# Optimization experiments

Hardware: AMD Instinct MI355X
Metric: run time of the kernel (lower is better)

## Reference

```python
import jax, jax.numpy as jnp
import numpy as np

N = 50000   # num nodes
E = 800000  # num edges
D = 128     # in_features
C = 1.0     # curvature c
MIN_NORM = 1e-15
BALL_EPS = 4e-3  # float32 boundary eps in PoincareBall.proj


def setup_inputs() -> dict:
    key = jax.random.key(0)
    k1, k2 = jax.random.split(key)
    x = jax.random.normal(k1, (N, D), dtype=jnp.float32)
    edge_index = jax.random.randint(k2, (2, E), 0, N, dtype=jnp.int32)
    return {"x": x, "edge_index": edge_index}


def _expmap0(u, c):
    sqrt_c = c ** 0.5
    u_norm = jnp.maximum(jnp.linalg.norm(u, axis=-1, keepdims=True), MIN_NORM)
    return jnp.tanh(sqrt_c * u_norm) * u / (sqrt_c * u_norm)


def _proj(p, c):
    norm = jnp.maximum(jnp.linalg.norm(p, axis=-1, keepdims=True), MIN_NORM)
    maxnorm = (1.0 - BALL_EPS) / (c ** 0.5)
    return jnp.where(norm > maxnorm, p / norm * maxnorm, p)


def reference(x, edge_index):
    row, col = edge_index[0], edge_index[1]
    # add_remaining_self_loops: drop existing self-loops (weight->0), append N fresh self-loops w=1
    w = jnp.where(row == col, 0.0, 1.0).astype(x.dtype)
    loop = jnp.arange(N, dtype=row.dtype)
    row_f = jnp.concatenate([row, loop])
    col_f = jnp.concatenate([col, loop])
    w_f = jnp.concatenate([w, jnp.ones((N,), x.dtype)])
    # symmetric GCN normalization: D^{-1/2} A D^{-1/2}
    deg = jax.ops.segment_sum(w_f, row_f, num_segments=N)
    dis = jnp.where(deg > 0, 1.0 / jnp.sqrt(jnp.where(deg > 0, deg, 1.0)), 0.0)
    nw = dis[row_f] * w_f * dis[col_f]  # [E+N]
    # gather source features, weighted scatter-add into destination rows
    support = nw[:, None] * x[col_f]                       # [E+N, D]
    result = jax.ops.segment_sum(support, row_f, num_segments=N)  # [N, D]
    return _proj(_expmap0(result, C), C)
```

## Files before the change

### kernel.cpp

```cpp
#include <hip/hip_runtime.h>
#include <math.h>

#define N_NODES 50000
#define N_EDGES 800000
#define DFEAT   128
#define MAXNORM (1.0f - 4e-3f)
#define CAP     32
#define OVF_CAP 8192
#define NPART   8
#define PSIZE   (N_NODES / NPART)
#define SENT    N_NODES

typedef float vfloat4 __attribute__((ext_vector_type(4)));


__device__ __forceinline__ void build_edge(int r, int c, int lo, int hi,
                                           int* __restrict__ deg,
                                           unsigned short* __restrict__ adj16,
                                           int* __restrict__ ovf, int* __restrict__ ovf_cnt) {
    if (r < lo || r >= hi || r == c) return;
    int pos = atomicAdd(&deg[r], 1);
    if (pos < CAP) adj16[r * CAP + pos] = (unsigned short)c;
    else {
        int o = atomicAdd(ovf_cnt, 1);
        if (o < OVF_CAP) { ovf[2 * o] = r; ovf[2 * o + 1] = c; }
    }
}

__global__ void k_build(const int* __restrict__ row, const int* __restrict__ col,
                        int* __restrict__ deg, unsigned short* __restrict__ adj16,
                        int* __restrict__ ovf, int* __restrict__ ovf_cnt, int e) {
    int p      = blockIdx.x & (NPART - 1);
    int vblock = blockIdx.x >> 3;
    int tpp    = (gridDim.x >> 3) * blockDim.x;
    int tid    = vblock * blockDim.x + threadIdx.x;
    int lo = p * PSIZE, hi = lo + PSIZE;

    int e4 = e >> 2;
    const int4* __restrict__ row4 = (const int4*)row;
    const int4* __restrict__ col4 = (const int4*)col;
    for (int i = tid; i < e4; i += tpp) {
        int4 r4 = row4[i];
        int4 c4 = col4[i];
        build_edge(r4.x, c4.x, lo, hi, deg, adj16, ovf, ovf_cnt);
        build_edge(r4.y, c4.y, lo, hi, deg, adj16, ovf, ovf_cnt);
        build_edge(r4.z, c4.z, lo, hi, deg, adj16, ovf, ovf_cnt);
        build_edge(r4.w, c4.w, lo, hi, deg, adj16, ovf, ovf_cnt);
    }
    for (int i = (e4 << 2) + tid; i < e; i += tpp)
        build_edge(row[i], col[i], lo, hi, deg, adj16, ovf, ovf_cnt);
}

__global__ __launch_bounds__(256) void k_prep(const float* __restrict__ x,
                                              const int* __restrict__ deg,
                                              unsigned int* __restrict__ xb,
                                              int nthreads) {
    int t = blockIdx.x * blockDim.x + threadIdx.x;
    if (t >= nthreads) return;

    int node = t >> 4;
    int part = t & 15;
    unsigned int w[4];
    if (node < N_NODES) {
        float dis = rsqrtf((float)(deg[node] + 1));
        const vfloat4* x4 = (const vfloat4*)(x + (size_t)node * DFEAT + part * 8);
        vfloat4 a = __builtin_nontemporal_load(x4);
        vfloat4 b = __builtin_nontemporal_load(x4 + 1);
        float fs[8] = {a.x, a.y, a.z, a.w, b.x, b.y, b.z, b.w};
        #pragma unroll
        for (int k = 0; k < 4; ++k) {
            unsigned int lo = __float_as_uint(fs[2 * k] * dis);
            unsigned int hi = __float_as_uint(fs[2 * k + 1] * dis);
            lo = (lo + 0x7FFFu + ((lo >> 16) & 1u)) >> 16;
            hi = (hi + 0x7FFFu + ((hi >> 16) & 1u)) >> 16;
            w[k] = lo | (hi << 16);
        }
    } else {
        w[0] = w[1] = w[2] = w[3] = 0u;
    }
    ((uint4*)xb)[t] = make_uint4(w[0], w[1], w[2], w[3]);
}

__device__ __forceinline__ float bf_lo(unsigned int w) { return __uint_as_float(w << 16); }
__device__ __forceinline__ float bf_hi(unsigned int w) { return __uint_as_float(w & 0xFFFF0000u); }

__global__ __launch_bounds__(256) void k_gather_bf(const unsigned int* __restrict__ xb,
                                                   const unsigned short* __restrict__ adj16,
                                                   const int* __restrict__ deg,
                                                   const int* __restrict__ ovf,
                                                   const int* __restrict__ ovf_cnt,
                                                   float* __restrict__ out, int n) {
    int lane = threadIdx.x & 63;
    int half = lane >> 5;
    int fl   = lane & 31;
    int rowi = blockIdx.x * 4 + (threadIdx.x >> 6);
    if (rowi >= n) return;

    int cnt    = deg[rowi];
    int capcnt = cnt < CAP ? cnt : CAP;

    int a = SENT;
    if (lane < capcnt) a = (int)adj16[rowi * CAP + lane];

    const unsigned int* __restrict__ xw = xb + 2 * fl;

    uint2 sv = *(const uint2*)(xw + rowi * (DFEAT / 2));

    float acc0 = 0.f, acc1 = 0.f, acc2 = 0.f, acc3 = 0.f;

    {
        int c[8];
        #pragma unroll
        for (int j = 0; j < 8; ++j) c[j] = __shfl(a, 2 * j + half);
        uint2 v[8];
        #pragma unroll
        for (int j = 0; j < 8; ++j) v[j] = *(const uint2*)(xw + c[j] * (DFEAT / 2));
        #pragma unroll
        for (int j = 0; j < 8; ++j) {
            acc0 += bf_lo(v[j].x); acc1 += bf_hi(v[j].x);
            acc2 += bf_lo(v[j].y); acc3 += bf_hi(v[j].y);
        }
    }
    if (capcnt > 16) {
        int c[8];
        #pragma unroll
        for (int j = 0; j < 8; ++j) c[j] = __shfl(a, 16 + 2 * j + half);
        uint2 v[8];
        #pragma unroll
        for (int j = 0; j < 8; ++j) v[j] = *(const uint2*)(xw + c[j] * (DFEAT / 2));
        #pragma unroll
        for (int j = 0; j < 8; ++j) {
            acc0 += bf_lo(v[j].x); acc1 += bf_hi(v[j].x);
            acc2 += bf_lo(v[j].y); acc3 += bf_hi(v[j].y);
        }
    }

    if (cnt > CAP && half == 0) {
        int novf = *ovf_cnt;
        for (int k = 0; k < novf; ++k) {
            if (ovf[2 * k] == rowi) {
                uint2 v = *(const uint2*)(xw + ovf[2 * k + 1] * (DFEAT / 2));
                acc0 += bf_lo(v.x); acc1 += bf_hi(v.x);
                acc2 += bf_lo(v.y); acc3 += bf_hi(v.y);
            }
        }
    }

    acc0 += __shfl_xor(acc0, 32);
    acc1 += __shfl_xor(acc1, 32);
    acc2 += __shfl_xor(acc2, 32);
    acc3 += __shfl_xor(acc3, 32);

    acc0 += bf_lo(sv.x); acc1 += bf_hi(sv.x);
    acc2 += bf_lo(sv.y); acc3 += bf_hi(sv.y);

    float di = rsqrtf((float)(cnt + 1));
    acc0 *= di; acc1 *= di; acc2 *= di; acc3 *= di;

    float nsq = acc0 * acc0 + acc1 * acc1 + acc2 * acc2 + acc3 * acc3;
    #pragma unroll
    for (int off = 16; off > 0; off >>= 1) nsq += __shfl_xor(nsq, off);

    float un = fmaxf(sqrtf(nsq), 1e-15f);
    float th = tanhf(un);
    float scale = th / un;
    if (th > MAXNORM) scale *= MAXNORM / th;

    if (half == 0) {
        vfloat4 o = { acc0 * scale, acc1 * scale, acc2 * scale, acc3 * scale };
        __builtin_nontemporal_store(o, (vfloat4*)(out + (size_t)rowi * DFEAT + 4 * fl));
    }
}


#define SCAN_BLK 256
#define NUM_SCAN_BLOCKS ((N_NODES + SCAN_BLK - 1) / SCAN_BLK)

__global__ void k_init_deg(int* __restrict__ deg, int n) {
    int i = blockIdx.x * blockDim.x + threadIdx.x;
    if (i < n) deg[i] = 1;
}

__global__ void k_hist(const int* __restrict__ row, const int* __restrict__ col,
                       int* __restrict__ deg, int e) {
    int i = blockIdx.x * blockDim.x + threadIdx.x;
    if (i < e) {
        int r = row[i], c = col[i];
        if (r != c) atomicAdd(&deg[r], 1);
    }
}

__global__ __launch_bounds__(SCAN_BLK) void k_block_sums(const int* __restrict__ deg,
                                                         int* __restrict__ blockSums, int n) {
    __shared__ int s[SCAN_BLK];
    int t = threadIdx.x;
    int i = blockIdx.x * SCAN_BLK + t;
    s[t] = (i < n) ? (deg[i] - 1) : 0;
    __syncthreads();
    for (int off = SCAN_BLK / 2; off > 0; off >>= 1) {
        if (t < off) s[t] += s[t + off];
        __syncthreads();
    }
    if (t == 0) blockSums[blockIdx.x] = s[0];
}

__global__ __launch_bounds__(SCAN_BLK) void k_scan_blocks(const int* __restrict__ blockSums,
                                                          int* __restrict__ blockBase) {
    __shared__ int s[SCAN_BLK];
    int t = threadIdx.x;
    s[t] = (t < NUM_SCAN_BLOCKS) ? blockSums[t] : 0;
    __syncthreads();
    for (int off = 1; off < SCAN_BLK; off <<= 1) {
        int v = (t >= off) ? s[t - off] : 0;
        __syncthreads();
        s[t] += v;
        __syncthreads();
    }
    if (t < NUM_SCAN_BLOCKS) blockBase[t] = (t == 0) ? 0 : s[t - 1];
}

__global__ __launch_bounds__(SCAN_BLK) void k_block_scan(const int* __restrict__ deg,
                                                         const int* __restrict__ blockBase,
                                                         int* __restrict__ offs,
                                                         int* __restrict__ cursor, int n) {
    __shared__ int s[SCAN_BLK];
    int t = threadIdx.x;
    int i = blockIdx.x * SCAN_BLK + t;
    int cnt = (i < n) ? (deg[i] - 1) : 0;
    s[t] = cnt;
    __syncthreads();
    for (int off = 1; off < SCAN_BLK; off <<= 1) {
        int v = (t >= off) ? s[t - off] : 0;
        __syncthreads();
        s[t] += v;
        __syncthreads();
    }
    if (i < n) {
        int excl = s[t] - cnt + blockBase[blockIdx.x];
        offs[i]   = excl;
        cursor[i] = excl;
    }
}

__global__ void k_scatter(const int* __restrict__ row, const int* __restrict__ col,
                          int* __restrict__ cursor, int* __restrict__ adj, int e) {
    int i = blockIdx.x * blockDim.x + threadIdx.x;
    if (i < e) {
        int r = row[i], c = col[i];
        if (r != c) {
            int pos = atomicAdd(&cursor[r], 1);
            adj[pos] = c;
        }
    }
}

__global__ __launch_bounds__(256) void k_gather_csr(const float* __restrict__ x,
                                                    const int* __restrict__ adj,
                                                    const int* __restrict__ offs,
                                                    const int* __restrict__ deg,
                                                    float* __restrict__ out, int n) {
    int lane = threadIdx.x & 63;
    int rowi = blockIdx.x * 4 + (threadIdx.x >> 6);
    if (rowi >= n) return;

    const float2* __restrict__ x2 = (const float2*)x;
    int beg = offs[rowi];
    int cnt = deg[rowi] - 1;

    float2 acc = make_float2(0.0f, 0.0f);
    for (int base = 0; base < cnt; base += 64) {
        int m = cnt - base; if (m > 64) m = 64;
        int a = 0;
        if (lane < m) a = adj[beg + base + lane];
        for (int nb = 0; nb < m; ++nb) {
            int c = __shfl(a, nb);
            float w = rsqrtf((float)deg[c]);
            float2 v = x2[c * (DFEAT / 2) + lane];
            acc.x += w * v.x;
            acc.y += w * v.y;
        }
    }
    float di = rsqrtf((float)deg[rowi]);
    float2 self = x2[rowi * (DFEAT / 2) + lane];
    acc.x = di * (acc.x + di * self.x);
    acc.y = di * (acc.y + di * self.y);

    float nsq = acc.x * acc.x + acc.y * acc.y;
    #pragma unroll
    for (int off = 32; off > 0; off >>= 1) nsq += __shfl_xor(nsq, off);

    float un = fmaxf(sqrtf(nsq), 1e-15f);
    float th = tanhf(un);
    float scale = th / un;
    if (th > MAXNORM) scale *= MAXNORM / th;

    float2 o = make_float2(acc.x * scale, acc.y * scale);
    ((float2*)out)[rowi * (DFEAT / 2) + lane] = o;
}


extern "C" void kernel_launch(void* const* d_in, const int* in_sizes, int n_in,
                              void* d_out, int out_size, void* d_ws, size_t ws_size,
                              hipStream_t stream) {
    const float* x          = (const float*)d_in[0];
    const int*   edge_index = (const int*)d_in[1];
    const int*   row = edge_index;
    const int*   col = edge_index + N_EDGES;
    float* out = (float*)d_out;
    char*  ws  = (char*)d_ws;

    size_t sz_xb    = sizeof(unsigned short) * (size_t)(N_NODES + 1) * DFEAT;
    size_t sz_adj16 = sizeof(unsigned short) * (size_t)N_NODES * CAP;
    size_t sz_deg   = sizeof(int) * (size_t)N_NODES;
    size_t need = sz_xb + sz_adj16 + sz_deg + sizeof(int) * (1 + 2 * (size_t)OVF_CAP);

    dim3 blk(256);
    if (ws_size >= need) {
        size_t off = 0;
        unsigned int*   xb      = (unsigned int*)(ws + off);   off += sz_xb;
        unsigned short* adj16   = (unsigned short*)(ws + off); off += sz_adj16;
        int*            deg     = (int*)(ws + off);            off += sz_deg;
        int*            ovf_cnt = (int*)(ws + off);            off += sizeof(int);
        int*            ovf     = (int*)(ws + off);

        int nprep = (N_NODES + 1) * (DFEAT / 8);
        hipMemsetAsync(deg, 0, sz_deg + sizeof(int), stream);
        k_build<<<dim3(8192), blk, 0, stream>>>(row, col, deg, adj16, ovf, ovf_cnt, N_EDGES);
        k_prep<<<dim3((nprep + 255) / 256), blk, 0, stream>>>(x, deg, xb, nprep);
        k_gather_bf<<<dim3((N_NODES + 3) / 4), blk, 0, stream>>>(xb, adj16, deg, ovf, ovf_cnt, out, N_NODES);
    } else {
        size_t off = 0;
        int* deg       = (int*)(ws + off); off += sizeof(int) * (size_t)N_NODES;
        int* offs      = (int*)(ws + off); off += sizeof(int) * (size_t)N_NODES;
        int* cursor    = (int*)(ws + off); off += sizeof(int) * (size_t)N_NODES;
        int* blockSums = (int*)(ws + off); off += sizeof(int) * (size_t)NUM_SCAN_BLOCKS;
        int* blockBase = (int*)(ws + off); off += sizeof(int) * (size_t)NUM_SCAN_BLOCKS;
        int* adj       = (int*)(ws + off);

        k_init_deg<<<dim3((N_NODES + 255) / 256), blk, 0, stream>>>(deg, N_NODES);
        k_hist<<<dim3((N_EDGES + 255) / 256), blk, 0, stream>>>(row, col, deg, N_EDGES);
        k_block_sums<<<dim3(NUM_SCAN_BLOCKS), dim3(SCAN_BLK), 0, stream>>>(deg, blockSums, N_NODES);
        k_scan_blocks<<<dim3(1), dim3(SCAN_BLK), 0, stream>>>(blockSums, blockBase);
        k_block_scan<<<dim3(NUM_SCAN_BLOCKS), dim3(SCAN_BLK), 0, stream>>>(deg, blockBase, offs, cursor, N_NODES);
        k_scatter<<<dim3((N_EDGES + 255) / 256), blk, 0, stream>>>(row, col, cursor, adj, N_EDGES);
        k_gather_csr<<<dim3((N_NODES + 3) / 4), blk, 0, stream>>>(x, adj, offs, deg, out, N_NODES);
    }
}
```

Measured before the change: 152.8 us.

## Fuse bf16 conversion into build kernel and apply source-degree weights in gather

```diff
diff --git a/kernel.cpp b/kernel.cpp
--- a/kernel.cpp
+++ b/kernel.cpp
@@ -27,9 +27,37 @@
     }
 }
 
-__global__ void k_build(const int* __restrict__ row, const int* __restrict__ col,
-                        int* __restrict__ deg, unsigned short* __restrict__ adj16,
-                        int* __restrict__ ovf, int* __restrict__ ovf_cnt, int e) {
+__global__ void k_build_conv(const int* __restrict__ row, const int* __restrict__ col,
+                             const float* __restrict__ x,
+                             int* __restrict__ deg, unsigned short* __restrict__ adj16,
+                             unsigned int* __restrict__ xb,
+                             int* __restrict__ ovf, int* __restrict__ ovf_cnt,
+                             int e, int nprep) {
+    int gtid = blockIdx.x * blockDim.x + threadIdx.x;
+    int nthr = gridDim.x * blockDim.x;
+    for (int t = gtid; t < nprep; t += nthr) {
+        int node = t >> 4;
+        int part = t & 15;
+        unsigned int w[4];
+        if (node < N_NODES) {
+            const vfloat4* x4 = (const vfloat4*)(x + (size_t)node * DFEAT + part * 8);
+            vfloat4 a = __builtin_nontemporal_load(x4);
+            vfloat4 b = __builtin_nontemporal_load(x4 + 1);
+            float fs[8] = {a.x, a.y, a.z, a.w, b.x, b.y, b.z, b.w};
+            #pragma unroll
+            for (int k = 0; k < 4; ++k) {
+                unsigned int lo = __float_as_uint(fs[2 * k]);
+                unsigned int hi = __float_as_uint(fs[2 * k + 1]);
+                lo = (lo + 0x7FFFu + ((lo >> 16) & 1u)) >> 16;
+                hi = (hi + 0x7FFFu + ((hi >> 16) & 1u)) >> 16;
+                w[k] = lo | (hi << 16);
+            }
+        } else {
+            w[0] = w[1] = w[2] = w[3] = 0u;
+        }
+        ((uint4*)xb)[t] = make_uint4(w[0], w[1], w[2], w[3]);
+    }
+
     int p      = blockIdx.x & (NPART - 1);
     int vblock = blockIdx.x >> 3;
     int tpp    = (gridDim.x >> 3) * blockDim.x;
@@ -49,36 +77,6 @@
     }
     for (int i = (e4 << 2) + tid; i < e; i += tpp)
         build_edge(row[i], col[i], lo, hi, deg, adj16, ovf, ovf_cnt);
-}
-
-__global__ __launch_bounds__(256) void k_prep(const float* __restrict__ x,
-                                              const int* __restrict__ deg,
-                                              unsigned int* __restrict__ xb,
-                                              int nthreads) {
-    int t = blockIdx.x * blockDim.x + threadIdx.x;
-    if (t >= nthreads) return;
-
-    int node = t >> 4;
-    int part = t & 15;
-    unsigned int w[4];
-    if (node < N_NODES) {
-        float dis = rsqrtf((float)(deg[node] + 1));
-        const vfloat4* x4 = (const vfloat4*)(x + (size_t)node * DFEAT + part * 8);
-        vfloat4 a = __builtin_nontemporal_load(x4);
-        vfloat4 b = __builtin_nontemporal_load(x4 + 1);
-        float fs[8] = {a.x, a.y, a.z, a.w, b.x, b.y, b.z, b.w};
-        #pragma unroll
-        for (int k = 0; k < 4; ++k) {
-            unsigned int lo = __float_as_uint(fs[2 * k] * dis);
-            unsigned int hi = __float_as_uint(fs[2 * k + 1] * dis);
-            lo = (lo + 0x7FFFu + ((lo >> 16) & 1u)) >> 16;
-            hi = (hi + 0x7FFFu + ((hi >> 16) & 1u)) >> 16;
-            w[k] = lo | (hi << 16);
-        }
-    } else {
-        w[0] = w[1] = w[2] = w[3] = 0u;
-    }
-    ((uint4*)xb)[t] = make_uint4(w[0], w[1], w[2], w[3]);
 }
 
 __device__ __forceinline__ float bf_lo(unsigned int w) { return __uint_as_float(w << 16); }
@@ -113,12 +111,14 @@
         #pragma unroll
         for (int j = 0; j < 8; ++j) c[j] = __shfl(a, 2 * j + half);
         uint2 v[8];
-        #pragma unroll
-        for (int j = 0; j < 8; ++j) v[j] = *(const uint2*)(xw + c[j] * (DFEAT / 2));
+        int   d[8];
+        #pragma unroll
+        for (int j = 0; j < 8; ++j) { v[j] = *(const uint2*)(xw + c[j] * (DFEAT / 2)); d[j] = deg[c[j]]; }
         #pragma unroll
         for (int j = 0; j < 8; ++j) {
-            acc0 += bf_lo(v[j].x); acc1 += bf_hi(v[j].x);
-            acc2 += bf_lo(v[j].y); acc3 += bf_hi(v[j].y);
+            float wgt = rsqrtf((float)(d[j] + 1));
+            acc0 += wgt * bf_lo(v[j].x); acc1 += wgt * bf_hi(v[j].x);
+            acc2 += wgt * bf_lo(v[j].y); acc3 += wgt * bf_hi(v[j].y);
         }
     }
     if (capcnt > 16) {
@@ -126,12 +126,14 @@
         #pragma unroll
         for (int j = 0; j < 8; ++j) c[j] = __shfl(a, 16 + 2 * j + half);
         uint2 v[8];
-        #pragma unroll
-        for (int j = 0; j < 8; ++j) v[j] = *(const uint2*)(xw + c[j] * (DFEAT / 2));
+        int   d[8];
+        #pragma unroll
+        for (int j = 0; j < 8; ++j) { v[j] = *(const uint2*)(xw + c[j] * (DFEAT / 2)); d[j] = deg[c[j]]; }
         #pragma unroll
         for (int j = 0; j < 8; ++j) {
-            acc0 += bf_lo(v[j].x); acc1 += bf_hi(v[j].x);
-            acc2 += bf_lo(v[j].y); acc3 += bf_hi(v[j].y);
+            float wgt = rsqrtf((float)(d[j] + 1));
+            acc0 += wgt * bf_lo(v[j].x); acc1 += wgt * bf_hi(v[j].x);
+            acc2 += wgt * bf_lo(v[j].y); acc3 += wgt * bf_hi(v[j].y);
         }
     }
 
@@ -139,9 +141,11 @@
         int novf = *ovf_cnt;
         for (int k = 0; k < novf; ++k) {
             if (ovf[2 * k] == rowi) {
-                uint2 v = *(const uint2*)(xw + ovf[2 * k + 1] * (DFEAT / 2));
-                acc0 += bf_lo(v.x); acc1 += bf_hi(v.x);
-                acc2 += bf_lo(v.y); acc3 += bf_hi(v.y);
+                int cc = ovf[2 * k + 1];
+                uint2 v = *(const uint2*)(xw + cc * (DFEAT / 2));
+                float wgt = rsqrtf((float)(deg[cc] + 1));
+                acc0 += wgt * bf_lo(v.x); acc1 += wgt * bf_hi(v.x);
+                acc2 += wgt * bf_lo(v.y); acc3 += wgt * bf_hi(v.y);
             }
         }
     }
@@ -151,10 +155,11 @@
     acc2 += __shfl_xor(acc2, 32);
     acc3 += __shfl_xor(acc3, 32);
 
-    acc0 += bf_lo(sv.x); acc1 += bf_hi(sv.x);
-    acc2 += bf_lo(sv.y); acc3 += bf_hi(sv.y);
-
     float di = rsqrtf((float)(cnt + 1));
+
+    acc0 += di * bf_lo(sv.x); acc1 += di * bf_hi(sv.x);
+    acc2 += di * bf_lo(sv.y); acc3 += di * bf_hi(sv.y);
+
     acc0 *= di; acc1 *= di; acc2 *= di; acc3 *= di;
 
     float nsq = acc0 * acc0 + acc1 * acc1 + acc2 * acc2 + acc3 * acc3;
@@ -325,8 +330,7 @@
 
         int nprep = (N_NODES + 1) * (DFEAT / 8);
         hipMemsetAsync(deg, 0, sz_deg + sizeof(int), stream);
-        k_build<<<dim3(8192), blk, 0, stream>>>(row, col, deg, adj16, ovf, ovf_cnt, N_EDGES);
-        k_prep<<<dim3((nprep + 255) / 256), blk, 0, stream>>>(x, deg, xb, nprep);
+        k_build_conv<<<dim3(8192), blk, 0, stream>>>(row, col, x, deg, adj16, xb, ovf, ovf_cnt, N_EDGES, nprep);
         k_gather_bf<<<dim3((N_NODES + 3) / 4), blk, 0, stream>>>(xb, adj16, deg, ovf, ovf_cnt, out, N_NODES);
     } else {
         size_t off = 0;
```

Result: no change. 150.9 us, median of 3 (-1.3%).
